# Kernel optimization log

Hardware: AMD Instinct MI355X
Metric: run time of the kernel (lower is better)

Reference implementation:

```python
import jax, jax.numpy as jnp
import numpy as np

GH, GW = 16, 16          # group_size
DIM = 512
H = 8                    # num_heads
PD = DIM // 16           # pos_dim = (dim//4)//4 = 32
B = 256                  # number of groups (batch*windows)
N = GH * GW


def _make_bias_tables():
    # biases buffer: all 2D relative offsets, shape [(2GH-1)*(2GW-1), 2]
    h = np.arange(1 - GH, GH)
    w = np.arange(1 - GW, GW)
    bh, bw = np.meshgrid(h, w, indexing='ij')
    biases = np.stack([bh, bw]).reshape(2, -1).T.astype(np.float32)
    # relative_position_index: [N, N] lookup into the bias table
    ch, cw = np.meshgrid(np.arange(GH), np.arange(GW), indexing='ij')
    coords = np.stack([ch, cw]).reshape(2, -1)            # [2, N]
    rel = coords[:, :, None] - coords[:, None, :]         # [2, N, N]
    rel = rel.transpose(1, 2, 0).copy()                   # [N, N, 2]
    rel[:, :, 0] += GH - 1
    rel[:, :, 1] += GW - 1
    rel[:, :, 0] *= 2 * GW - 1
    idx = rel.sum(-1)
    return biases, idx.astype(np.int32)


def _ln(x, g, b, eps=1e-5):
    m = x.mean(-1, keepdims=True)
    v = ((x - m) ** 2).mean(-1, keepdims=True)
    return (x - m) / jnp.sqrt(v + eps) * g + b


def setup_inputs() -> dict:
    key = jax.random.key(0)
    ks = jax.random.split(key, 16)
    s = 0.02
    biases_np, idx_np = _make_bias_tables()
    return {
        'x': jax.random.normal(ks[0], (B, N, DIM), dtype=jnp.float32),
        'qkv_w': jax.random.normal(ks[1], (DIM, 3 * DIM), dtype=jnp.float32) * s,
        'qkv_b': jnp.zeros((3 * DIM,), jnp.float32),
        'proj_w': jax.random.normal(ks[2], (DIM, DIM), dtype=jnp.float32) * s,
        'proj_b': jnp.zeros((DIM,), jnp.float32),
        'p1_w': jax.random.normal(ks[3], (2, PD), dtype=jnp.float32) * s,
        'p1_b': jnp.zeros((PD,), jnp.float32),
        'g1': jnp.ones((PD,), jnp.float32), 'b1': jnp.zeros((PD,), jnp.float32),
        'p2_w': jax.random.normal(ks[4], (PD, PD), dtype=jnp.float32) * s,
        'p2_b': jnp.zeros((PD,), jnp.float32),
        'g2': jnp.ones((PD,), jnp.float32), 'b2': jnp.zeros((PD,), jnp.float32),
        'p3_w': jax.random.normal(ks[5], (PD, PD), dtype=jnp.float32) * s,
        'p3_b': jnp.zeros((PD,), jnp.float32),
        'g3': jnp.ones((PD,), jnp.float32), 'b3': jnp.zeros((PD,), jnp.float32),
        'p4_w': jax.random.normal(ks[6], (PD, H), dtype=jnp.float32) * s,
        'p4_b': jnp.zeros((H,), jnp.float32),
        'biases': jnp.asarray(biases_np),
        'rel_idx': jnp.asarray(idx_np),
    }


def reference(x, qkv_w, qkv_b, proj_w, proj_b,
              p1_w, p1_b, g1, b1, p2_w, p2_b, g2, b2,
              p3_w, p3_b, g3, b3, p4_w, p4_b, biases, rel_idx):
    Bn, Nn, C = x.shape
    hd = C // H
    scale = hd ** -0.5
    qkv = (x @ qkv_w + qkv_b).reshape(Bn, Nn, 3, H, hd).transpose(2, 0, 3, 1, 4)
    q, k, v = qkv[0] * scale, qkv[1], qkv[2]      # [B, H, N, hd]
    attn = jnp.einsum('bhnd,bhmd->bhnm', q, k)    # [B, H, N, N]
    # dynamic position bias MLP on the offset table
    h1 = jax.nn.relu(_ln(biases @ p1_w + p1_b, g1, b1))
    h2 = jax.nn.relu(_ln(h1 @ p2_w + p2_b, g2, b2))
    h3 = jax.nn.relu(_ln(h2 @ p3_w + p3_b, g3, b3))
    pos = h3 @ p4_w + p4_b                        # [L, H]
    rpb = pos[rel_idx.reshape(-1)].reshape(Nn, Nn, H).transpose(2, 0, 1)  # [H, N, N]
    attn = jax.nn.softmax(attn + rpb[None], axis=-1)
    out = jnp.einsum('bhnm,bhmd->bhnd', attn, v)
    out = out.transpose(0, 2, 1, 3).reshape(Bn, Nn, C)
    return out @ proj_w + proj_b
```

## Files before the change

### kernel.cpp

```cpp
#include <hip/hip_runtime.h>
#include <stdint.h>

typedef __bf16 bf16x8 __attribute__((ext_vector_type(8)));
typedef float  f32x4  __attribute__((ext_vector_type(4)));
typedef unsigned short ushort_t;

#define MFMA16(a,b,c) __builtin_amdgcn_mfma_f32_16x16x32_bf16((a),(b),(c),0,0,0)

#define GLOAD16(gsrc, ldst) \
    __builtin_amdgcn_global_load_lds((const __attribute__((address_space(1))) void*)(gsrc), \
                                     (__attribute__((address_space(3))) void*)(ldst), 16, 0, 0)

#define BATCH 256
#define NTOK  256
#define DIM   512
#define NH    8
#define HD    64
#define PD    32
#define LTAB  961

#define POS_OFF   0
#define RPB_OFF   32768
#define WQKV_OFF  (RPB_OFF + 2097152)
#define WPROJ_OFF (WQKV_OFF + 1572864)
#define QKV_OFF   (WPROJ_OFF + 524288)
#define AOUT_OFF  (QKV_OFF + 201326592)
#define XB_OFF    AOUT_OFF

__device__ __forceinline__ ushort_t f2bf(float f) {
    unsigned int u = __builtin_bit_cast(unsigned int, f);
    u += 0x7FFFu + ((u >> 16) & 1u);
    return (ushort_t)(u >> 16);
}

__global__ __launch_bounds__(256) void convert_x(
    const float* __restrict__ x, ushort_t* __restrict__ xb)
{
    size_t i = ((size_t)blockIdx.x * 256 + threadIdx.x) * 8;
    float4 f0 = *(const float4*)(x + i);
    float4 f1 = *(const float4*)(x + i + 4);
    uint4 o;
    o.x = (unsigned)f2bf(f0.x) | ((unsigned)f2bf(f0.y) << 16);
    o.y = (unsigned)f2bf(f0.z) | ((unsigned)f2bf(f0.w) << 16);
    o.z = (unsigned)f2bf(f1.x) | ((unsigned)f2bf(f1.y) << 16);
    o.w = (unsigned)f2bf(f1.z) | ((unsigned)f2bf(f1.w) << 16);
    *reinterpret_cast<uint4*>(xb + i) = o;
}

__global__ __launch_bounds__(256) void convert_w(
    const float* __restrict__ qkv_w, const float* __restrict__ proj_w,
    ushort_t* __restrict__ wqkvT, ushort_t* __restrict__ wprojT)
{
    int i = blockIdx.x * 256 + threadIdx.x;
    int n = i >> 9, k = i & 511;
    wqkvT[i] = f2bf(qkv_w[(size_t)k * 1536 + n]);
    if (i < 512 * 512) {
        int n2 = i >> 9, k2 = i & 511;
        wprojT[i] = f2bf(proj_w[(size_t)k2 * 512 + n2]);
    }
}

__device__ __forceinline__ float ln_relu_t(float h, int j,
                                           const float* __restrict__ g,
                                           const float* __restrict__ bb) {
    float m = h;
    m += __shfl_xor(m, 1); m += __shfl_xor(m, 2); m += __shfl_xor(m, 4);
    m += __shfl_xor(m, 8); m += __shfl_xor(m, 16);
    m *= (1.0f / PD);
    float d = h - m;
    float v = d * d;
    v += __shfl_xor(v, 1); v += __shfl_xor(v, 2); v += __shfl_xor(v, 4);
    v += __shfl_xor(v, 8); v += __shfl_xor(v, 16);
    v *= (1.0f / PD);
    float x = d * rsqrtf(v + 1e-5f) * g[j] + bb[j];
    return x > 0.f ? x : 0.f;
}

__global__ __launch_bounds__(256) void pos_mlp(
    const float* __restrict__ biases,
    const float* __restrict__ p1_w, const float* __restrict__ p1_b,
    const float* __restrict__ g1, const float* __restrict__ b1,
    const float* __restrict__ p2_w, const float* __restrict__ p2_b,
    const float* __restrict__ g2, const float* __restrict__ b2,
    const float* __restrict__ p3_w, const float* __restrict__ p3_b,
    const float* __restrict__ g3, const float* __restrict__ b3,
    const float* __restrict__ p4_w, const float* __restrict__ p4_b,
    float* __restrict__ pos)
{
    __shared__ float hs[8][33];
    int tid = threadIdx.x;
    int rl = tid >> 5, j = tid & 31;
    int r = blockIdx.x * 8 + rl;
    bool ok = r < LTAB;
    float c0 = ok ? biases[r * 2 + 0] : 0.f;
    float c1 = ok ? biases[r * 2 + 1] : 0.f;

    float h = c0 * p1_w[j] + c1 * p1_w[PD + j] + p1_b[j];
    h = ln_relu_t(h, j, g1, b1);

    hs[rl][j] = h;
    __syncthreads();
    float s = p2_b[j];
#pragma unroll
    for (int i = 0; i < PD; i++) s += hs[rl][i] * p2_w[i * PD + j];
    __syncthreads();
    h = ln_relu_t(s, j, g2, b2);

    hs[rl][j] = h;
    __syncthreads();
    s = p3_b[j];
#pragma unroll
    for (int i = 0; i < PD; i++) s += hs[rl][i] * p3_w[i * PD + j];
    __syncthreads();
    h = ln_relu_t(s, j, g3, b3);

    hs[rl][j] = h;
    __syncthreads();
    if (ok && j < NH) {
        float o = p4_b[j];
#pragma unroll
        for (int i = 0; i < PD; i++) o += hs[rl][i] * p4_w[i * NH + j];
        pos[r * NH + j] = o;
    }
}

__global__ __launch_bounds__(256) void rpb_gather(
    const float* __restrict__ pos, const int* __restrict__ rel_idx,
    float* __restrict__ rpb)
{
    int i = blockIdx.x * 256 + threadIdx.x;
    int idx = rel_idx[i];
#pragma unroll
    for (int hh = 0; hh < NH; hh++) rpb[(size_t)hh * 65536 + i] = pos[idx * NH + hh];
}

__global__ __launch_bounds__(256) void qkv_gemm(
    const ushort_t* __restrict__ xb, const ushort_t* __restrict__ wT,
    const float* __restrict__ qkv_b, ushort_t* __restrict__ qkvb)
{
    __shared__ ushort_t As[2][4096];
    __shared__ ushort_t Bs[2][4096];
    int t = threadIdx.x;
    int bid = blockIdx.x;
    int wgid = (bid & 7) * 768 + (bid >> 3);
    int mt = wgid / 12, nt = wgid % 12;
    int m0 = mt * 128, n0 = nt * 128;
    int lane = t & 63, w = t >> 6;
    int wm = w >> 1, wn = w & 1;
    int lr = lane & 15, lk = lane >> 4;
    int srow = lane >> 2, scol = (lane & 3) * 8;
    const ushort_t* Asrc = xb + (size_t)(m0 + srow) * 512 + scol;
    const ushort_t* Bsrc = wT + (size_t)(n0 + srow) * 512 + scol;

    f32x4 acc[4][4];
#pragma unroll
    for (int fr = 0; fr < 4; fr++)
#pragma unroll
        for (int fc = 0; fc < 4; fc++) acc[fr][fc] = (f32x4){0.f, 0.f, 0.f, 0.f};

#define QSTAGE(buf, kt) do { \
    _Pragma("unroll") \
    for (int i_ = 0; i_ < 2; i_++) { \
        int row_ = w * 32 + i_ * 16; \
        GLOAD16(Asrc + (size_t)row_ * 512 + (kt) * 32, &As[buf][row_ * 32]); \
        GLOAD16(Bsrc + (size_t)row_ * 512 + (kt) * 32, &Bs[buf][row_ * 32]); \
    } } while (0)

    QSTAGE(0, 0);
    asm volatile("s_waitcnt vmcnt(0)" ::: "memory");
    __syncthreads();
    int cur = 0;
    for (int kt = 0; kt < 16; ++kt) {
        if (kt < 15) QSTAGE(cur ^ 1, kt + 1);
        bf16x8 a[4], b[4];
#pragma unroll
        for (int fr = 0; fr < 4; fr++)
            a[fr] = *reinterpret_cast<const bf16x8*>(&As[cur][(wm * 64 + fr * 16 + lr) * 32 + lk * 8]);
#pragma unroll
        for (int fc = 0; fc < 4; fc++)
            b[fc] = *reinterpret_cast<const bf16x8*>(&Bs[cur][(wn * 64 + fc * 16 + lr) * 32 + lk * 8]);
#pragma unroll
        for (int fr = 0; fr < 4; fr++)
#pragma unroll
            for (int fc = 0; fc < 4; fc++)
                acc[fr][fc] = MFMA16(a[fr], b[fc], acc[fr][fc]);
        if (kt < 15) {
            asm volatile("s_waitcnt vmcnt(0)" ::: "memory");
            __syncthreads();
        }
        cur ^= 1;
    }
#undef QSTAGE

    int s = n0 >> 9;
    if (s < 2) {
        float sc = (s == 0) ? 0.125f : 1.0f;
#pragma unroll
        for (int fc = 0; fc < 4; fc++) {
            int n = n0 + wn * 64 + fc * 16 + lr;
            float bias = qkv_b[n];
            int hh = (n >> 6) & 7, d = n & 63;
#pragma unroll
            for (int fr = 0; fr < 4; fr++)
#pragma unroll
                for (int r = 0; r < 4; r++) {
                    int m = m0 + wm * 64 + fr * 16 + lk * 4 + r;
                    int bg = m >> 8, tok = m & 255;
                    float v = (acc[fr][fc][r] + bias) * sc;
                    qkvb[((((size_t)s * 256 + bg) * 8 + hh) * 256 + tok) * 64 + d] = f2bf(v);
                }
        }
    } else {
#pragma unroll
        for (int fc = 0; fc < 4; fc++) {
            int n = n0 + wn * 64 + fc * 16 + lr;
            float bias = qkv_b[n];
            int hh = (n >> 6) & 7, d = n & 63;
#pragma unroll
            for (int fr = 0; fr < 4; fr++) {
                int m = m0 + wm * 64 + fr * 16 + lk * 4;
                int bg = m >> 8, tok = m & 255;
                uint2 pk;
                pk.x = (unsigned)f2bf(acc[fr][fc][0] + bias) |
                       ((unsigned)f2bf(acc[fr][fc][1] + bias) << 16);
                pk.y = (unsigned)f2bf(acc[fr][fc][2] + bias) |
                       ((unsigned)f2bf(acc[fr][fc][3] + bias) << 16);
                *reinterpret_cast<uint2*>(
                    qkvb + ((((size_t)512 + bg) * 8 + hh) * 64 + d) * 256 + tok) = pk;
            }
        }
    }
}

__global__ __launch_bounds__(256) void attn_kernel(
    const ushort_t* __restrict__ qkvb, const float* __restrict__ rpb,
    ushort_t* __restrict__ aout)
{
    __shared__ ushort_t Ps[4][32][40];
    __shared__ ushort_t Os[4][16 * 72];
    int t = threadIdx.x, lane = t & 63, w = t >> 6;
    int bid = blockIdx.x;
    int qh = bid & 1; int bh = bid >> 1; int hh = bh & 7; int bg = bh >> 3;
    const ushort_t* Qg  = qkvb + (((size_t)bg * 8 + hh) * 256) * 64;
    const ushort_t* Kg  = qkvb + (((size_t)(256 + bg) * 8 + hh) * 256) * 64;
    const ushort_t* VTg = qkvb + (((size_t)(512 + bg) * 8 + hh) * 64) * 256;
    int lr = lane & 15, lk = lane >> 4;
    int qrow0 = qh * 128 + w * 32;

    bf16x8 qf[2][2];
#pragma unroll
    for (int fr = 0; fr < 2; fr++)
#pragma unroll
        for (int kc = 0; kc < 2; kc++)
            qf[fr][kc] = *reinterpret_cast<const bf16x8*>(
                Qg + (size_t)(qrow0 + fr * 16 + lr) * 64 + kc * 32 + lk * 8);

    f32x4 oacc[2][4];
    float rsum[2][4];
#pragma unroll
    for (int fr = 0; fr < 2; fr++) {
#pragma unroll
        for (int fc = 0; fc < 4; fc++) oacc[fr][fc] = (f32x4){0.f, 0.f, 0.f, 0.f};
#pragma unroll
        for (int r = 0; r < 4; r++) rsum[fr][r] = 0.f;
    }

    for (int kt = 0; kt < 8; ++kt) {
        f32x4 sacc[2][2];
#pragma unroll
        for (int fr = 0; fr < 2; fr++)
#pragma unroll
            for (int fc = 0; fc < 2; fc++) sacc[fr][fc] = (f32x4){0.f, 0.f, 0.f, 0.f};
#pragma unroll
        for (int kc = 0; kc < 2; kc++) {
            bf16x8 kb0 = *reinterpret_cast<const bf16x8*>(
                Kg + (size_t)(kt * 32 + lr) * 64 + kc * 32 + lk * 8);
            bf16x8 kb1 = *reinterpret_cast<const bf16x8*>(
                Kg + (size_t)(kt * 32 + 16 + lr) * 64 + kc * 32 + lk * 8);
            sacc[0][0] = MFMA16(qf[0][kc], kb0, sacc[0][0]);
            sacc[0][1] = MFMA16(qf[0][kc], kb1, sacc[0][1]);
            sacc[1][0] = MFMA16(qf[1][kc], kb0, sacc[1][0]);
            sacc[1][1] = MFMA16(qf[1][kc], kb1, sacc[1][1]);
        }
#pragma unroll
        for (int fr = 0; fr < 2; fr++)
#pragma unroll
            for (int fc = 0; fc < 2; fc++)
#pragma unroll
                for (int r = 0; r < 4; r++) {
                    int row = qrow0 + fr * 16 + lk * 4 + r;
                    int col = kt * 32 + fc * 16 + lr;
                    float lg = sacc[fr][fc][r] + rpb[((size_t)hh * 256 + row) * 256 + col];
                    float p = __expf(lg);
                    rsum[fr][r] += p;
                    Ps[w][fr * 16 + lk * 4 + r][fc * 16 + lr] = f2bf(p);
                }
        bf16x8 pa[2], vb[4];
#pragma unroll
        for (int fr = 0; fr < 2; fr++)
            pa[fr] = *reinterpret_cast<const bf16x8*>(&Ps[w][fr * 16 + lr][lk * 8]);
#pragma unroll
        for (int fc = 0; fc < 4; fc++)
            vb[fc] = *reinterpret_cast<const bf16x8*>(
                VTg + (size_t)(fc * 16 + lr) * 256 + kt * 32 + lk * 8);
#pragma unroll
        for (int fr = 0; fr < 2; fr++)
#pragma unroll
            for (int fc = 0; fc < 4; fc++)
                oacc[fr][fc] = MFMA16(pa[fr], vb[fc], oacc[fr][fc]);
    }
    float rinv[2][4];
#pragma unroll
    for (int fr = 0; fr < 2; fr++)
#pragma unroll
        for (int r = 0; r < 4; r++) {
            float s = rsum[fr][r];
            s += __shfl_xor(s, 1); s += __shfl_xor(s, 2);
            s += __shfl_xor(s, 4); s += __shfl_xor(s, 8);
            rinv[fr][r] = __frcp_rn(s);
        }
#pragma unroll
    for (int fr = 0; fr < 2; fr++) {
#pragma unroll
        for (int fc = 0; fc < 4; fc++)
#pragma unroll
            for (int r = 0; r < 4; r++)
                Os[w][(lk * 4 + r) * 72 + fc * 16 + lr] = f2bf(oacc[fr][fc][r] * rinv[fr][r]);
#pragma unroll
        for (int ii = 0; ii < 2; ii++) {
            int j = lane + ii * 64;
            int row = j >> 3, ch = j & 7;
            uint4 v = *reinterpret_cast<const uint4*>(&Os[w][row * 72 + ch * 8]);
            *reinterpret_cast<uint4*>(
                aout + ((size_t)(bg * 256 + qrow0 + fr * 16 + row)) * 512 + hh * 64 + ch * 8) = v;
        }
    }
}

__global__ __launch_bounds__(256) void proj_gemm(
    const ushort_t* __restrict__ ain, const ushort_t* __restrict__ wT,
    const float* __restrict__ proj_b, float* __restrict__ out)
{
    __shared__ ushort_t As[2][4096];
    __shared__ ushort_t Bs[2][4096];
    int t = threadIdx.x;
    int bid = blockIdx.x;
    int wgid = (bid & 7) * 256 + (bid >> 3);
    int mt = wgid / 4, nt = wgid % 4;
    int m0 = mt * 128, n0 = nt * 128;
    int lane = t & 63, w = t >> 6;
    int wm = w >> 1, wn = w & 1;
    int lr = lane & 15, lk = lane >> 4;
    int srow = lane >> 2, scol = (lane & 3) * 8;
    const ushort_t* Asrc = ain + (size_t)(m0 + srow) * 512 + scol;
    const ushort_t* Bsrc = wT + (size_t)(n0 + srow) * 512 + scol;
    f32x4 acc[4][4];
#pragma unroll
    for (int fr = 0; fr < 4; fr++)
#pragma unroll
        for (int fc = 0; fc < 4; fc++) acc[fr][fc] = (f32x4){0.f, 0.f, 0.f, 0.f};

#define PSTAGE(buf, kt) do { \
    _Pragma("unroll") \
    for (int i_ = 0; i_ < 2; i_++) { \
        int row_ = w * 32 + i_ * 16; \
        GLOAD16(Asrc + (size_t)row_ * 512 + (kt) * 32, &As[buf][row_ * 32]); \
        GLOAD16(Bsrc + (size_t)row_ * 512 + (kt) * 32, &Bs[buf][row_ * 32]); \
    } } while (0)

    PSTAGE(0, 0);
    asm volatile("s_waitcnt vmcnt(0)" ::: "memory");
    __syncthreads();
    int cur = 0;
    for (int kt = 0; kt < 16; ++kt) {
        if (kt < 15) PSTAGE(cur ^ 1, kt + 1);
        bf16x8 a[4], b[4];
#pragma unroll
        for (int fr = 0; fr < 4; fr++)
            a[fr] = *reinterpret_cast<const bf16x8*>(&As[cur][(wm * 64 + fr * 16 + lr) * 32 + lk * 8]);
#pragma unroll
        for (int fc = 0; fc < 4; fc++)
            b[fc] = *reinterpret_cast<const bf16x8*>(&Bs[cur][(wn * 64 + fc * 16 + lr) * 32 + lk * 8]);
#pragma unroll
        for (int fr = 0; fr < 4; fr++)
#pragma unroll
            for (int fc = 0; fc < 4; fc++)
                acc[fr][fc] = MFMA16(a[fr], b[fc], acc[fr][fc]);
        if (kt < 15) {
            asm volatile("s_waitcnt vmcnt(0)" ::: "memory");
            __syncthreads();
        }
        cur ^= 1;
    }
#undef PSTAGE
#pragma unroll
    for (int fc = 0; fc < 4; fc++) {
        int n = n0 + wn * 64 + fc * 16 + lr;
        float bias = proj_b[n];
#pragma unroll
        for (int fr = 0; fr < 4; fr++)
#pragma unroll
            for (int r = 0; r < 4; r++) {
                int m = m0 + wm * 64 + fr * 16 + lk * 4 + r;
                out[(size_t)m * 512 + n] = acc[fr][fc][r] + bias;
            }
    }
}

extern "C" void kernel_launch(void* const* d_in, const int* in_sizes, int n_in,
                              void* d_out, int out_size, void* d_ws, size_t ws_size,
                              hipStream_t stream) {
    const float* x      = (const float*)d_in[0];
    const float* qkv_w  = (const float*)d_in[1];
    const float* qkv_b  = (const float*)d_in[2];
    const float* proj_w = (const float*)d_in[3];
    const float* proj_b = (const float*)d_in[4];
    const float* p1_w = (const float*)d_in[5];
    const float* p1_b = (const float*)d_in[6];
    const float* g1   = (const float*)d_in[7];
    const float* b1   = (const float*)d_in[8];
    const float* p2_w = (const float*)d_in[9];
    const float* p2_b = (const float*)d_in[10];
    const float* g2   = (const float*)d_in[11];
    const float* b2   = (const float*)d_in[12];
    const float* p3_w = (const float*)d_in[13];
    const float* p3_b = (const float*)d_in[14];
    const float* g3   = (const float*)d_in[15];
    const float* b3   = (const float*)d_in[16];
    const float* p4_w = (const float*)d_in[17];
    const float* p4_b = (const float*)d_in[18];
    const float* biases  = (const float*)d_in[19];
    const int*   rel_idx = (const int*)d_in[20];
    float* out = (float*)d_out;

    char* ws = (char*)d_ws;
    float*    pos    = (float*)(ws + POS_OFF);
    float*    rpb    = (float*)(ws + RPB_OFF);
    ushort_t* wqkvT  = (ushort_t*)(ws + WQKV_OFF);
    ushort_t* wprojT = (ushort_t*)(ws + WPROJ_OFF);
    ushort_t* qkvb   = (ushort_t*)(ws + QKV_OFF);
    ushort_t* aoutb  = (ushort_t*)(ws + AOUT_OFF);
    ushort_t* xb     = (ushort_t*)(ws + XB_OFF);

    convert_x<<<dim3(16384), dim3(256), 0, stream>>>(x, xb);
    convert_w<<<dim3(3072), dim3(256), 0, stream>>>(qkv_w, proj_w, wqkvT, wprojT);
    pos_mlp<<<dim3(121), dim3(256), 0, stream>>>(biases, p1_w, p1_b, g1, b1,
                                                 p2_w, p2_b, g2, b2,
                                                 p3_w, p3_b, g3, b3,
                                                 p4_w, p4_b, pos);
    rpb_gather<<<dim3(256), dim3(256), 0, stream>>>(pos, rel_idx, rpb);
    qkv_gemm<<<dim3(512 * 12), dim3(256), 0, stream>>>(xb, wqkvT, qkv_b, qkvb);
    attn_kernel<<<dim3(4096), dim3(256), 0, stream>>>(qkvb, rpb, aoutb);
    proj_gemm<<<dim3(512 * 4), dim3(256), 0, stream>>>(aoutb, wprojT, proj_b, out);
}
```

Measured before the change: 446.2 us.

## Triple-buffer GEMM LDS stages with XOR swizzle and tiled weight transpose

Both the QKV and projection GEMMs move from double to triple-buffered LDS staging, keeping two global-to-LDS loads in flight (vmcnt(4)) so load latency overlaps better with MFMA work. The LDS column layout is XOR-swizzled on both the store and the fragment reads to cut bank conflicts. The weight conversion kernel is replaced by a shared-memory tiled transpose, so global reads and writes are coalesced. LDS use per block grows by half, which may lower occupancy, and the swizzle must match exactly between writer and reader.

```diff
diff --git a/kernel.cpp b/kernel.cpp
--- a/kernel.cpp
+++ b/kernel.cpp
@@ -47,16 +47,26 @@
     *reinterpret_cast<uint4*>(xb + i) = o;
 }
 
-__global__ __launch_bounds__(256) void convert_w(
-    const float* __restrict__ qkv_w, const float* __restrict__ proj_w,
-    ushort_t* __restrict__ wqkvT, ushort_t* __restrict__ wprojT)
-{
-    int i = blockIdx.x * 256 + threadIdx.x;
-    int n = i >> 9, k = i & 511;
-    wqkvT[i] = f2bf(qkv_w[(size_t)k * 1536 + n]);
-    if (i < 512 * 512) {
-        int n2 = i >> 9, k2 = i & 511;
-        wprojT[i] = f2bf(proj_w[(size_t)k2 * 512 + n2]);
+__global__ __launch_bounds__(256) void transpose_w(
+    const float* __restrict__ src, ushort_t* __restrict__ dst, int K, int Nn)
+{
+    __shared__ ushort_t tile[64][65];
+    int tiles_n = Nn >> 6;
+    int tn = blockIdx.x % tiles_n, tk = blockIdx.x / tiles_n;
+    int n0 = tn * 64, k0 = tk * 64;
+    int t = threadIdx.x;
+#pragma unroll
+    for (int i = 0; i < 16; i++) {
+        int idx = t + i * 256;
+        int kl = idx >> 6, nl = idx & 63;
+        tile[nl][kl] = f2bf(src[(size_t)(k0 + kl) * Nn + n0 + nl]);
+    }
+    __syncthreads();
+#pragma unroll
+    for (int i = 0; i < 16; i++) {
+        int idx = t + i * 256;
+        int nl = idx >> 6, kl = idx & 63;
+        dst[(size_t)(n0 + nl) * K + k0 + kl] = tile[nl][kl];
     }
 }
 
@@ -138,8 +148,8 @@
     const ushort_t* __restrict__ xb, const ushort_t* __restrict__ wT,
     const float* __restrict__ qkv_b, ushort_t* __restrict__ qkvb)
 {
-    __shared__ ushort_t As[2][4096];
-    __shared__ ushort_t Bs[2][4096];
+    __shared__ ushort_t As[3][4096];
+    __shared__ ushort_t Bs[3][4096];
     int t = threadIdx.x;
     int bid = blockIdx.x;
     int wgid = (bid & 7) * 768 + (bid >> 3);
@@ -148,9 +158,11 @@
     int lane = t & 63, w = t >> 6;
     int wm = w >> 1, wn = w & 1;
     int lr = lane & 15, lk = lane >> 4;
-    int srow = lane >> 2, scol = (lane & 3) * 8;
+    int srow = lane >> 2;
+    int scol = (((lane & 3) ^ ((lane >> 3) & 3)) << 3);
     const ushort_t* Asrc = xb + (size_t)(m0 + srow) * 512 + scol;
     const ushort_t* Bsrc = wT + (size_t)(n0 + srow) * 512 + scol;
+    int rx = ((lk ^ ((lr >> 1) & 3)) << 3);
 
     f32x4 acc[4][4];
 #pragma unroll
@@ -167,28 +179,32 @@
     } } while (0)
 
     QSTAGE(0, 0);
-    asm volatile("s_waitcnt vmcnt(0)" ::: "memory");
-    __syncthreads();
-    int cur = 0;
+    QSTAGE(1, 1);
+    asm volatile("s_waitcnt vmcnt(4)" ::: "memory");
+    __syncthreads();
+#pragma unroll
     for (int kt = 0; kt < 16; ++kt) {
-        if (kt < 15) QSTAGE(cur ^ 1, kt + 1);
+        int cb = kt % 3;
+        if (kt + 2 < 16) QSTAGE((kt + 2) % 3, kt + 2);
         bf16x8 a[4], b[4];
 #pragma unroll
         for (int fr = 0; fr < 4; fr++)
-            a[fr] = *reinterpret_cast<const bf16x8*>(&As[cur][(wm * 64 + fr * 16 + lr) * 32 + lk * 8]);
+            a[fr] = *reinterpret_cast<const bf16x8*>(&As[cb][(wm * 64 + fr * 16 + lr) * 32 + rx]);
 #pragma unroll
         for (int fc = 0; fc < 4; fc++)
-            b[fc] = *reinterpret_cast<const bf16x8*>(&Bs[cur][(wn * 64 + fc * 16 + lr) * 32 + lk * 8]);
+            b[fc] = *reinterpret_cast<const bf16x8*>(&Bs[cb][(wn * 64 + fc * 16 + lr) * 32 + rx]);
 #pragma unroll
         for (int fr = 0; fr < 4; fr++)
 #pragma unroll
             for (int fc = 0; fc < 4; fc++)
                 acc[fr][fc] = MFMA16(a[fr], b[fc], acc[fr][fc]);
-        if (kt < 15) {
+        if (kt + 2 < 16) {
+            asm volatile("s_waitcnt vmcnt(4)" ::: "memory");
+            __syncthreads();
+        } else if (kt + 1 < 16) {
             asm volatile("s_waitcnt vmcnt(0)" ::: "memory");
             __syncthreads();
         }
-        cur ^= 1;
     }
 #undef QSTAGE
 
@@ -341,8 +357,8 @@
     const ushort_t* __restrict__ ain, const ushort_t* __restrict__ wT,
     const float* __restrict__ proj_b, float* __restrict__ out)
 {
-    __shared__ ushort_t As[2][4096];
-    __shared__ ushort_t Bs[2][4096];
+    __shared__ ushort_t As[3][4096];
+    __shared__ ushort_t Bs[3][4096];
     int t = threadIdx.x;
     int bid = blockIdx.x;
     int wgid = (bid & 7) * 256 + (bid >> 3);
@@ -351,9 +367,11 @@
     int lane = t & 63, w = t >> 6;
     int wm = w >> 1, wn = w & 1;
     int lr = lane & 15, lk = lane >> 4;
-    int srow = lane >> 2, scol = (lane & 3) * 8;
+    int srow = lane >> 2;
+    int scol = (((lane & 3) ^ ((lane >> 3) & 3)) << 3);
     const ushort_t* Asrc = ain + (size_t)(m0 + srow) * 512 + scol;
     const ushort_t* Bsrc = wT + (size_t)(n0 + srow) * 512 + scol;
+    int rx = ((lk ^ ((lr >> 1) & 3)) << 3);
     f32x4 acc[4][4];
 #pragma unroll
     for (int fr = 0; fr < 4; fr++)
@@ -369,28 +387,32 @@
     } } while (0)
 
     PSTAGE(0, 0);
-    asm volatile("s_waitcnt vmcnt(0)" ::: "memory");
-    __syncthreads();
-    int cur = 0;
+    PSTAGE(1, 1);
+    asm volatile("s_waitcnt vmcnt(4)" ::: "memory");
+    __syncthreads();
+#pragma unroll
     for (int kt = 0; kt < 16; ++kt) {
-        if (kt < 15) PSTAGE(cur ^ 1, kt + 1);
+        int cb = kt % 3;
+        if (kt + 2 < 16) PSTAGE((kt + 2) % 3, kt + 2);
         bf16x8 a[4], b[4];
 #pragma unroll
         for (int fr = 0; fr < 4; fr++)
-            a[fr] = *reinterpret_cast<const bf16x8*>(&As[cur][(wm * 64 + fr * 16 + lr) * 32 + lk * 8]);
+            a[fr] = *reinterpret_cast<const bf16x8*>(&As[cb][(wm * 64 + fr * 16 + lr) * 32 + rx]);
 #pragma unroll
         for (int fc = 0; fc < 4; fc++)
-            b[fc] = *reinterpret_cast<const bf16x8*>(&Bs[cur][(wn * 64 + fc * 16 + lr) * 32 + lk * 8]);
+            b[fc] = *reinterpret_cast<const bf16x8*>(&Bs[cb][(wn * 64 + fc * 16 + lr) * 32 + rx]);
 #pragma unroll
         for (int fr = 0; fr < 4; fr++)
 #pragma unroll
             for (int fc = 0; fc < 4; fc++)
                 acc[fr][fc] = MFMA16(a[fr], b[fc], acc[fr][fc]);
-        if (kt < 15) {
+        if (kt + 2 < 16) {
+            asm volatile("s_waitcnt vmcnt(4)" ::: "memory");
+            __syncthreads();
+        } else if (kt + 1 < 16) {
             asm volatile("s_waitcnt vmcnt(0)" ::: "memory");
             __syncthreads();
         }
-        cur ^= 1;
     }
 #undef PSTAGE
 #pragma unroll
@@ -443,7 +465,8 @@
     ushort_t* xb     = (ushort_t*)(ws + XB_OFF);
 
     convert_x<<<dim3(16384), dim3(256), 0, stream>>>(x, xb);
-    convert_w<<<dim3(3072), dim3(256), 0, stream>>>(qkv_w, proj_w, wqkvT, wprojT);
+    transpose_w<<<dim3(24 * 8), dim3(256), 0, stream>>>(qkv_w, wqkvT, 512, 1536);
+    transpose_w<<<dim3(8 * 8), dim3(256), 0, stream>>>(proj_w, wprojT, 512, 512);
     pos_mlp<<<dim3(121), dim3(256), 0, stream>>>(biases, p1_w, p1_b, g1, b1,
                                                  p2_w, p2_b, g2, b2,
                                                  p3_w, p3_b, g3, b3,
```

Result: faster. 429.9 us (-3.6%).
